# Performance work log

Hardware: AMD Instinct MI355X
Metric: run time of the kernel (lower is better)

The kernel has to match this reference:

```python
import jax, jax.numpy as jnp
import numpy as np

RADIUS = 5          # box-filter radius -> 11x11 kernel
TEMP = 0.5          # multinomial temperature
NSAMP = 5           # sampling_num
EPS = 1e-6
BN_EPS = 1e-5


def _conv(x, w, stride=1, padding=0, groups=1):
    return jax.lax.conv_general_dilated(
        x, w, window_strides=(stride, stride),
        padding=[(padding, padding), (padding, padding)],
        feature_group_count=groups,
        dimension_numbers=("NCHW", "OIHW", "NCHW"))


def custom_conv(x, w, key, stride=1, padding=0):
    """conv2d with cosine-activation regularization (bias=False path)."""
    B = x.shape[0]
    Cout = w.shape[0]
    # all-ones 'norm' conv on x*x
    x_norm = jnp.sqrt(_conv(x * x, jnp.ones_like(w), stride, padding))
    y = _conv(x, w, stride, padding)
    w_norm = jnp.sqrt(jnp.sum(w * w, axis=(1, 2, 3)))  # per-out-channel Frobenius norm
    cosine = y / (w_norm[None, :, None, None] + EPS) / (x_norm + EPS)
    # 11x11 depthwise box filter
    k = 2 * RADIUS + 1
    dw = jnp.ones((Cout, 1, k, k), x.dtype)
    cosine_mean = _conv(cosine, dw, 1, RADIUS, groups=Cout) / (k * k)
    H, W = cosine.shape[2], cosine.shape[3]
    # multinomial(NSAMP, exp(cosine/TEMP)) counts, no_grad in original
    logits = jax.lax.stop_gradient(cosine).reshape(B, Cout, H * W) / TEMP
    idx = jax.random.categorical(key, logits, axis=-1, shape=(NSAMP, B, Cout))
    bi = jnp.broadcast_to(jnp.arange(B)[None, :, None], (NSAMP, B, Cout))
    ci = jnp.broadcast_to(jnp.arange(Cout)[None, None, :], (NSAMP, B, Cout))
    mask = jnp.zeros((B, Cout, H * W), x.dtype).at[bi, ci, idx].add(1.0)
    cm = cosine_mean.reshape(B, Cout, H * W)
    act = ((mask * cm).sum(-1) / mask.sum(-1)).mean()
    return y, act


def batchnorm(x, g, b):
    # training-mode batch statistics (biased variance), like nn.BatchNorm2d
    m = x.mean(axis=(0, 2, 3), keepdims=True)
    v = x.var(axis=(0, 2, 3), keepdims=True)
    return (x - m) / jnp.sqrt(v + BN_EPS) * g[None, :, None, None] + b[None, :, None, None]


def setup_inputs() -> dict:
    key = jax.random.key(0)
    ks = jax.random.split(key, 10)
    x = jax.random.normal(ks[0], (16, 256, 56, 56), jnp.float32)
    w1 = jax.random.normal(ks[1], (64, 256, 1, 1), jnp.float32) * 0.05
    w2 = jax.random.normal(ks[2], (64, 64, 3, 3), jnp.float32) * 0.05
    w3 = jax.random.normal(ks[3], (256, 64, 1, 1), jnp.float32) * 0.05
    g1 = 1.0 + 0.05 * jax.random.normal(ks[4], (64,), jnp.float32)
    b1 = 0.05 * jax.random.normal(ks[5], (64,), jnp.float32)
    g2 = 1.0 + 0.05 * jax.random.normal(ks[6], (64,), jnp.float32)
    b2 = 0.05 * jax.random.normal(ks[7], (64,), jnp.float32)
    g3 = 1.0 + 0.05 * jax.random.normal(ks[8], (256,), jnp.float32)
    b3 = 0.05 * jax.random.normal(ks[9], (256,), jnp.float32)
    return {"x": x, "w1": w1, "w2": w2, "w3": w3,
            "g1": g1, "b1": b1, "g2": g2, "b2": b2, "g3": g3, "b3": b3}


def reference(x, w1, w2, w3, g1, b1, g2, b2, g3, b3):
    k0, k1, k2 = jax.random.split(jax.random.key(42), 3)
    acc = jnp.asarray(0.0, x.dtype)
    out, a = custom_conv(x, w1, k0)           # conv1x1
    acc = acc + a
    out = jax.nn.relu(batchnorm(out, g1, b1))
    out, a = custom_conv(out, w2, k1, padding=1)  # conv3x3, stride 1
    acc = acc + a
    out = jax.nn.relu(batchnorm(out, g2, b2))
    out, a = custom_conv(out, w3, k2)         # conv1x1 expand
    acc = acc + a
    out = batchnorm(out, g3, b3)
    out = jax.nn.relu(out + x)                # identity shortcut (downsample=None)
    return out, acc
```

## Files before the change

kernel.cpp:

```cpp
#include <hip/hip_runtime.h>
#include <stdint.h>
#include <math.h>

#define HW 3136
#define NPIX 50176

typedef __attribute__((ext_vector_type(8))) short bf16x8;
typedef __attribute__((ext_vector_type(4))) float f32x4;
#define MFMA16(a, b, c) __builtin_amdgcn_mfma_f32_16x16x32_bf16(a, b, c, 0, 0, 0)

__device__ __forceinline__ unsigned short f2bf(float f) {
  unsigned u = __float_as_uint(f);
  u = (u + 0x7fffu + ((u >> 16) & 1u)) >> 16;
  return (unsigned short)u;
}
__device__ __forceinline__ unsigned pk2(float a, float b) {
  return (unsigned)f2bf(a) | ((unsigned)f2bf(b) << 16);
}
__device__ __forceinline__ float bf2f(unsigned short h) {
  return __uint_as_float(((unsigned)h) << 16);
}

#define ROTL32(v, r) __builtin_rotateleft32((uint32_t)(v), (r))

__host__ __device__ inline void threefry2x32(uint32_t k0, uint32_t k1,
                                             uint32_t x0, uint32_t x1,
                                             uint32_t& o0, uint32_t& o1) {
  uint32_t k2 = k0 ^ k1 ^ 0x1BD11BDAu;
  x0 += k0; x1 += k1;
  x0 += x1; x1 = ROTL32(x1, 13); x1 ^= x0;
  x0 += x1; x1 = ROTL32(x1, 15); x1 ^= x0;
  x0 += x1; x1 = ROTL32(x1, 26); x1 ^= x0;
  x0 += x1; x1 = ROTL32(x1, 6);  x1 ^= x0;
  x0 += k1; x1 += k2 + 1u;
  x0 += x1; x1 = ROTL32(x1, 17); x1 ^= x0;
  x0 += x1; x1 = ROTL32(x1, 29); x1 ^= x0;
  x0 += x1; x1 = ROTL32(x1, 16); x1 ^= x0;
  x0 += x1; x1 = ROTL32(x1, 24); x1 ^= x0;
  x0 += k2; x1 += k0 + 2u;
  x0 += x1; x1 = ROTL32(x1, 13); x1 ^= x0;
  x0 += x1; x1 = ROTL32(x1, 15); x1 ^= x0;
  x0 += x1; x1 = ROTL32(x1, 26); x1 ^= x0;
  x0 += x1; x1 = ROTL32(x1, 6);  x1 ^= x0;
  x0 += k0; x1 += k1 + 3u;
  x0 += x1; x1 = ROTL32(x1, 17); x1 ^= x0;
  x0 += x1; x1 = ROTL32(x1, 29); x1 ^= x0;
  x0 += x1; x1 = ROTL32(x1, 16); x1 ^= x0;
  x0 += x1; x1 = ROTL32(x1, 24); x1 ^= x0;
  x0 += k1; x1 += k2 + 4u;
  x0 += x1; x1 = ROTL32(x1, 13); x1 ^= x0;
  x0 += x1; x1 = ROTL32(x1, 15); x1 ^= x0;
  x0 += x1; x1 = ROTL32(x1, 26); x1 ^= x0;
  x0 += x1; x1 = ROTL32(x1, 6);  x1 ^= x0;
  x0 += k2; x1 += k0 + 5u;
  o0 = x0; o1 = x1;
}

#define TF5_R(r)                                            \
  _Pragma("unroll") for (int i = 0; i < 5; ++i) {           \
    x0[i] += x1[i]; x1[i] = ROTL32(x1[i], r) ^ x0[i];       \
  }
#define TF5_INJ(a, b)                                       \
  _Pragma("unroll") for (int i = 0; i < 5; ++i) {           \
    x0[i] += (a); x1[i] += (b);                             \
  }
__device__ __forceinline__ void threefry5(uint32_t k0, uint32_t k1,
    const uint32_t xa[5], const uint32_t xb[5], uint32_t oa[5], uint32_t ob[5]) {
  uint32_t k2 = k0 ^ k1 ^ 0x1BD11BDAu;
  uint32_t x0[5], x1[5];
  #pragma unroll
  for (int i = 0; i < 5; ++i) { x0[i] = xa[i] + k0; x1[i] = xb[i] + k1; }
  TF5_R(13) TF5_R(15) TF5_R(26) TF5_R(6)  TF5_INJ(k1, k2 + 1u)
  TF5_R(17) TF5_R(29) TF5_R(16) TF5_R(24) TF5_INJ(k2, k0 + 2u)
  TF5_R(13) TF5_R(15) TF5_R(26) TF5_R(6)  TF5_INJ(k0, k1 + 3u)
  TF5_R(17) TF5_R(29) TF5_R(16) TF5_R(24) TF5_INJ(k1, k2 + 4u)
  TF5_R(13) TF5_R(15) TF5_R(26) TF5_R(6)  TF5_INJ(k2, k0 + 5u)
  #pragma unroll
  for (int i = 0; i < 5; ++i) { oa[i] = x0[i]; ob[i] = x1[i]; }
}

#define NLN2F -0.6931471805599453f
#define NEG2LOG2E -2.8853900817779268f
__device__ __forceinline__ float exp_draw(uint32_t bits) {
  float u = __uint_as_float((bits >> 9) | 0x3f800000u) - 1.0f;
  u = fmaxf(u, 1.17549435e-38f);
  return NLN2F * __log2f(u);
}

template <int NT>
__device__ void sample5_body(const unsigned short* __restrict__ CS,
    float* __restrict__ acc, uint32_t key0, uint32_t key1, int BC, float scale,
    int u, unsigned* kmin, float* wsum) {
  const int v = u + (BC >> 1);
  const uint32_t sC = (uint32_t)BC * (uint32_t)HW;
  const uint32_t halfn = sC * 2u + (sC >> 1);
  const unsigned short* rowU = CS + (size_t)u * HW;
  const unsigned short* rowV = CS + (size_t)v * HW;
  const int tid = threadIdx.x;
  const int lane = tid & 63;

  if (tid < 10) { kmin[tid] = 0xFFFFFFFFu; wsum[tid] = 0.f; }

  unsigned bk[10];
  #pragma unroll
  for (int k = 0; k < 10; ++k) bk[k] = 0xFFFFFFFFu;

  const uint32_t baseU0 = (uint32_t)u * (uint32_t)HW;
  const uint32_t baseV0 = (uint32_t)v * (uint32_t)HW;
  for (int p = tid; p < HW; p += NT) {
    float wu = __builtin_amdgcn_exp2f(bf2f(rowU[p]) * NEG2LOG2E);
    float wv = __builtin_amdgcn_exp2f(bf2f(rowV[p]) * NEG2LOG2E);
    uint32_t eU = baseU0 + (uint32_t)p;
    uint32_t eV = baseV0 + (uint32_t)p;
    uint32_t xa[5] = {eU, eU + sC, eU + 2 * sC, eV, eV + sC};
    uint32_t xb[5] = {eU + halfn, eU + sC + halfn, eU + 2 * sC + halfn,
                      eV + halfn, eV + sC + halfn};
    uint32_t oa[5], ob[5];
    threefry5(key0, key1, xa, xb, oa, ob);
    uint32_t wds[10] = {oa[0], oa[1], oa[2], ob[3], ob[4],
                        oa[3], oa[4], ob[0], ob[1], ob[2]};
    #pragma unroll
    for (int k = 0; k < 10; ++k) {
      float s = exp_draw(wds[k]) * (k < 5 ? wu : wv);
      unsigned key = (__float_as_uint(s) & 0xFFFFF000u) | (unsigned)p;
      bk[k] = bk[k] < key ? bk[k] : key;
    }
  }

  __syncthreads();
  #pragma unroll
  for (int k = 0; k < 10; ++k) {
    unsigned kv = bk[k];
    #pragma unroll
    for (int o = 32; o; o >>= 1) {
      unsigned ov = __shfl_xor(kv, o);
      kv = kv < ov ? kv : ov;
    }
    if (lane == 0) atomicMin(&kmin[k], kv);
  }
  __syncthreads();

  for (int idx = tid; idx < 1210; idx += NT) {
    int win = idx / 121, j = idx - win * 121;
    int bidx = (int)(kmin[win] & 0xFFFu);
    int py = bidx / 56, px = bidx % 56;
    int yy = py + j / 11 - 5, xx = px + j % 11 - 5;
    if (yy >= 0 && yy < 56 && xx >= 0 && xx < 56) {
      const unsigned short* row = (win < 5) ? rowU : rowV;
      atomicAdd(&wsum[win], bf2f(row[yy * 56 + xx]));
    }
  }
  __syncthreads();
  if (tid == 0) {
    float t = 0.f;
    #pragma unroll
    for (int k = 0; k < 10; ++k) t += wsum[k];
    atomicAdd(acc, t * scale);
  }
}

template <int NT>
__global__ __launch_bounds__(NT) void sample5_k(const unsigned short* __restrict__ CS,
    float* __restrict__ acc, uint32_t key0, uint32_t key1, int BC, float scale) {
  __shared__ unsigned kmin[10];
  __shared__ float wsum[10];
  sample5_body<NT>(CS, acc, key0, key1, BC, scale, blockIdx.x, kmin, wsum);
}

template <int NT>
__device__ void sample5_half_argmin(const unsigned short* __restrict__ CS,
    uint32_t key0, uint32_t key1, int BC, int u, int half,
    unsigned* __restrict__ outk, unsigned* kmin) {
  const int v = u + (BC >> 1);
  const uint32_t sC = (uint32_t)BC * (uint32_t)HW;
  const uint32_t halfn = sC * 2u + (sC >> 1);
  const unsigned short* rowU = CS + (size_t)u * HW;
  const unsigned short* rowV = CS + (size_t)v * HW;
  const int tid = threadIdx.x;
  const int lane = tid & 63;

  if (tid < 10) kmin[tid] = 0xFFFFFFFFu;

  unsigned bk[10];
  #pragma unroll
  for (int k = 0; k < 10; ++k) bk[k] = 0xFFFFFFFFu;

  const uint32_t baseU0 = (uint32_t)u * (uint32_t)HW;
  const uint32_t baseV0 = (uint32_t)v * (uint32_t)HW;
  const int pEnd = (half + 1) * (HW / 2);
  for (int p = half * (HW / 2) + tid; p < pEnd; p += NT) {
    float wu = __builtin_amdgcn_exp2f(bf2f(rowU[p]) * NEG2LOG2E);
    float wv = __builtin_amdgcn_exp2f(bf2f(rowV[p]) * NEG2LOG2E);
    uint32_t eU = baseU0 + (uint32_t)p;
    uint32_t eV = baseV0 + (uint32_t)p;
    uint32_t xa[5] = {eU, eU + sC, eU + 2 * sC, eV, eV + sC};
    uint32_t xb[5] = {eU + halfn, eU + sC + halfn, eU + 2 * sC + halfn,
                      eV + halfn, eV + sC + halfn};
    uint32_t oa[5], ob[5];
    threefry5(key0, key1, xa, xb, oa, ob);
    uint32_t wds[10] = {oa[0], oa[1], oa[2], ob[3], ob[4],
                        oa[3], oa[4], ob[0], ob[1], ob[2]};
    #pragma unroll
    for (int k = 0; k < 10; ++k) {
      float s = exp_draw(wds[k]) * (k < 5 ? wu : wv);
      unsigned key = (__float_as_uint(s) & 0xFFFFF000u) | (unsigned)p;
      bk[k] = bk[k] < key ? bk[k] : key;
    }
  }

  __syncthreads();
  #pragma unroll
  for (int k = 0; k < 10; ++k) {
    unsigned kv = bk[k];
    #pragma unroll
    for (int o = 32; o; o >>= 1) {
      unsigned ov = __shfl_xor(kv, o);
      kv = kv < ov ? kv : ov;
    }
    if (lane == 0) atomicMin(&kmin[k], kv);
  }
  __syncthreads();
  if (tid < 10) outk[tid] = kmin[tid];
}

__device__ __forceinline__ void final_chunk(int chunk,
    const unsigned short* __restrict__ Y3, const float* __restrict__ X,
    const float* __restrict__ sc, const float* __restrict__ sh,
    float* __restrict__ out) {
  size_t i = ((size_t)chunk * 256 + threadIdx.x) * 4;
  int c = (int)((i / HW) % 256);
  float a = sc[c], d = sh[c];
  uint2 yd = *(const uint2*)&Y3[i];
  float4 xv = *(const float4*)&X[i];
  float4 r;
  r.x = fmaxf(0.f, fmaf(bf2f((unsigned short)(yd.x & 0xffff)), a, d) + xv.x);
  r.y = fmaxf(0.f, fmaf(bf2f((unsigned short)(yd.x >> 16)),    a, d) + xv.y);
  r.z = fmaxf(0.f, fmaf(bf2f((unsigned short)(yd.y & 0xffff)), a, d) + xv.z);
  r.w = fmaxf(0.f, fmaf(bf2f((unsigned short)(yd.y >> 16)),    a, d) + xv.w);
  *(float4*)&out[i] = r;
}

__global__ __launch_bounds__(256, 8) void mega_argmin_k(
    const unsigned short* __restrict__ CS1, const unsigned short* __restrict__ CS2,
    const unsigned short* __restrict__ CS3,
    const unsigned short* __restrict__ Y3, const float* __restrict__ X,
    const float* __restrict__ sc, const float* __restrict__ sh,
    float* __restrict__ out, unsigned* __restrict__ bkmin,
    uint32_t A0, uint32_t A1, uint32_t A2, uint32_t B0, uint32_t B1, uint32_t B2,
    int pairStart, int finb) {
  __shared__ unsigned kmin[10];
  const int g = blockIdx.x;
  if (g < finb)
    for (int cc = g; cc < 12544; cc += finb)
      final_chunk(cc, Y3, X, sc, sh, out);
  const int lp = g >> 1, half = g & 1;
  const int pi = pairStart + lp;
  const unsigned short* CSp; int u; uint32_t k0, k1; int BC;
  if (pi < 512)       { CSp = CS1; u = pi;        k0 = A0; k1 = A1; BC = 1024; }
  else if (pi < 1024) { CSp = CS2; u = pi - 512;  k0 = A2; k1 = B0; BC = 1024; }
  else                { CSp = CS3; u = pi - 1024; k0 = B1; k1 = B2; BC = 4096; }
  sample5_half_argmin<256>(CSp, k0, k1, BC, u, half, bkmin + (size_t)g * 10, kmin);
}

__global__ __launch_bounds__(256) void combine_k(
    const unsigned short* __restrict__ CS1, const unsigned short* __restrict__ CS2,
    const unsigned short* __restrict__ CS3,
    const unsigned* __restrict__ bkmin, float* __restrict__ psum,
    float s64, float s256, int pairStart) {
  __shared__ unsigned kmin[10];
  __shared__ float wsum[10];
  const int tid = threadIdx.x, lane = tid & 63, wv = tid >> 6;
  const int rp = blockIdx.x;
  const int pi = pairStart + rp;
  const unsigned short* rowU; const unsigned short* rowV; float scale;
  if (pi < 512) {
    rowU = CS1 + (size_t)pi * HW; rowV = CS1 + (size_t)(pi + 512) * HW; scale = s64;
  } else if (pi < 1024) {
    int u = pi - 512;
    rowU = CS2 + (size_t)u * HW; rowV = CS2 + (size_t)(u + 512) * HW; scale = s64;
  } else {
    int u = pi - 1024;
    rowU = CS3 + (size_t)u * HW; rowV = CS3 + (size_t)(u + 2048) * HW; scale = s256;
  }
  if (tid < 10) {
    unsigned a = bkmin[(size_t)(2 * rp) * 10 + tid];
    unsigned b = bkmin[(size_t)(2 * rp + 1) * 10 + tid];
    kmin[tid] = a < b ? a : b;
  }
  __syncthreads();
  for (int win = wv; win < 10; win += 4) {
    int bidx = (int)(kmin[win] & 0xFFFu);
    int py = bidx / 56, px = bidx % 56;
    const unsigned short* row = (win < 5) ? rowU : rowV;
    float s = 0.f;
    for (int j = lane; j < 121; j += 64) {
      int yy = py + j / 11 - 5, xx = px + j % 11 - 5;
      if (yy >= 0 && yy < 56 && xx >= 0 && xx < 56)
        s += bf2f(row[yy * 56 + xx]);
    }
    #pragma unroll
    for (int o = 32; o; o >>= 1) s += __shfl_xor(s, o);
    if (lane == 0) wsum[win] = s;
  }
  __syncthreads();
  if (tid == 0) {
    float t = 0.f;
    #pragma unroll
    for (int k = 0; k < 10; ++k) t += wsum[k];
    psum[rp] = t * scale;
  }
}

__global__ __launch_bounds__(256) void acc_write_k(const float* __restrict__ psum,
    const float* __restrict__ acc, float* __restrict__ out, int n) {
  __shared__ float W[4];
  const int tid = threadIdx.x, lane = tid & 63, wv = tid >> 6;
  float s = 0.f;
  for (int i = tid; i < n; i += 256) s += psum[i];
  #pragma unroll
  for (int o = 32; o; o >>= 1) s += __shfl_xor(s, o);
  if (lane == 0) W[wv] = s;
  __syncthreads();
  if (tid == 0) out[12845056] = W[0] + W[1] + W[2] + W[3] + acc[0];
}

__global__ void wprep_k(const float* __restrict__ w1, const float* __restrict__ w2,
                        const float* __restrict__ w3, float* __restrict__ invwn,
                        unsigned short* __restrict__ W1b, unsigned short* __restrict__ W2tb,
                        unsigned short* __restrict__ W3b) {
  int i = blockIdx.x * 256 + threadIdx.x;
  if (i < 16384) {
    W1b[i] = f2bf(w1[i]);
  } else if (i < 53248) {
    int o = i - 16384;
    int co = o / 576, r = o % 576, tap = r >> 6, ci = r & 63;
    W2tb[o] = f2bf(w2[co * 576 + ci * 9 + tap]);
  } else if (i < 69632) {
    int o = i - 53248;
    W3b[o] = f2bf(w3[o]);
  } else {
    int t = i - 69632;
    if (t < 64) {
      float s = 0.f;
      for (int k = 0; k < 256; k++) { float v = w1[t * 256 + k]; s = fmaf(v, v, s); }
      invwn[t] = 1.0f / (sqrtf(s) + 1e-6f);
    } else if (t < 128) {
      int c = t - 64; float s = 0.f;
      for (int k = 0; k < 576; k++) { float v = w2[c * 576 + k]; s = fmaf(v, v, s); }
      invwn[t] = 1.0f / (sqrtf(s) + 1e-6f);
    } else if (t < 384) {
      int c = t - 128; float s = 0.f;
      for (int k = 0; k < 64; k++) { float v = w3[c * 64 + k]; s = fmaf(v, v, s); }
      invwn[t] = 1.0f / (sqrtf(s) + 1e-6f);
    }
  }
}

__global__ __launch_bounds__(256) void bn_fin(const float* __restrict__ Sp,
    const float* __restrict__ Qp, const float* __restrict__ g,
    const float* __restrict__ b, float* __restrict__ sc, float* __restrict__ sh,
    int nblk) {
  const int c = blockIdx.x, tid = threadIdx.x;
  const float* rs = Sp + (size_t)c * nblk;
  const float* rq = Qp + (size_t)c * nblk;
  float s = 0.f, q = 0.f;
  for (int i = tid; i < nblk; i += 256) { s += rs[i]; q += rq[i]; }
  #pragma unroll
  for (int o = 32; o; o >>= 1) { s += __shfl_xor(s, o); q += __shfl_xor(q, o); }
  __shared__ float S[4], Q[4];
  int lane = tid & 63, wave = tid >> 6;
  if (lane == 0) { S[wave] = s; Q[wave] = q; }
  __syncthreads();
  if (tid == 0) {
    float st = S[0] + S[1] + S[2] + S[3];
    float qt = Q[0] + Q[1] + Q[2] + Q[3];
    float mean = st * (1.0f / (float)NPIX);
    float var = qt * (1.0f / (float)NPIX) - mean * mean;
    float sv = g[c] / sqrtf(var + 1e-5f);
    sc[c] = sv; sh[c] = b[c] - mean * sv;
  }
}

__global__ __launch_bounds__(256) void conv1_mfma(
    const float* __restrict__ X, const unsigned short* __restrict__ Wb,
    const float* __restrict__ invwn, unsigned short* __restrict__ Y1,
    unsigned short* __restrict__ CS, float* __restrict__ Sp, float* __restrict__ Qp) {
#define ST1 264
#define NB1 784
  __shared__ __align__(16) unsigned short bq[64 * ST1];
  __shared__ float sqp[4][64];
  __shared__ float ixn[64];
  const int p0 = blockIdx.x * 64, b = blockIdx.y;
  const int bid = b * 49 + blockIdx.x;
  const int tid = threadIdx.x;
  const int lane = tid & 63, wave = tid >> 6;
  const int m = lane & 15, quad = lane >> 4;
  const int co0 = wave * 16;
  const float* Xb = X + (size_t)b * 256 * HW + p0;

  bf16x8 afr[8];
  const unsigned short* wrow = Wb + (co0 + m) * 256 + quad * 8;
  #pragma unroll
  for (int k = 0; k < 8; ++k) afr[k] = *(const bf16x8*)(wrow + k * 32);

  {
    const int px = tid & 63, rg = tid >> 6;
    float sq = 0.f;
    #pragma unroll
    for (int it = 0; it < 16; ++it) {
      int ci = rg * 64 + it * 4;
      float v0 = Xb[(size_t)(ci + 0) * HW + px];
      float v1 = Xb[(size_t)(ci + 1) * HW + px];
      float v2 = Xb[(size_t)(ci + 2) * HW + px];
      float v3 = Xb[(size_t)(ci + 3) * HW + px];
      sq += v0 * v0 + v1 * v1 + v2 * v2 + v3 * v3;
      *(uint2*)&bq[px * ST1 + ci] = make_uint2(pk2(v0, v1), pk2(v2, v3));
    }
    sqp[rg][px] = sq;
  }
  __syncthreads();
  if (tid < 64)
    ixn[tid] = 1.0f / (sqrtf(sqp[0][tid] + sqp[1][tid] + sqp[2][tid] + sqp[3][tid]) + 1e-6f);
  __syncthreads();

  f32x4 acc[4];
  #pragma unroll
  for (int nt = 0; nt < 4; ++nt) acc[nt] = (f32x4)0.f;
  #pragma unroll
  for (int nt = 0; nt < 4; ++nt) {
    const unsigned short* brow = &bq[(nt * 16 + m) * ST1 + quad * 8];
    #pragma unroll
    for (int k = 0; k < 8; ++k) {
      bf16x8 bfrag = *(const bf16x8*)(brow + k * 32);
      acc[nt] = MFMA16(afr[k], bfrag, acc[nt]);
    }
  }

  float s[4] = {0, 0, 0, 0}, q[4] = {0, 0, 0, 0};
  #pragma unroll
  for (int nt = 0; nt < 4; ++nt) {
    int px = nt * 16 + m;
    size_t bp = (size_t)b * HW + p0 + px;
    float ix = ixn[px];
    *(uint2*)&Y1[bp * 64 + co0 + quad * 4] =
        make_uint2(pk2(acc[nt][0], acc[nt][1]), pk2(acc[nt][2], acc[nt][3]));
    #pragma unroll
    for (int r = 0; r < 4; ++r) {
      int co = co0 + quad * 4 + r;
      float v = acc[nt][r];
      CS[((size_t)b * 64 + co) * HW + p0 + px] = f2bf(v * invwn[co] * ix);
      s[r] += v; q[r] = fmaf(v, v, q[r]);
    }
  }
  #pragma unroll
  for (int r = 0; r < 4; ++r) {
    float ss = s[r], qq = q[r];
    #pragma unroll
    for (int o = 8; o; o >>= 1) { ss += __shfl_xor(ss, o); qq += __shfl_xor(qq, o); }
    if (m == 0) {
      int co = co0 + quad * 4 + r;
      Sp[(size_t)co * NB1 + bid] = ss; Qp[(size_t)co * NB1 + bid] = qq;
    }
  }
#undef NB1
#undef ST1
}

__global__ __launch_bounds__(256) void conv2_mfma(
    const unsigned short* __restrict__ Y1, const unsigned short* __restrict__ W2tb,
    const float* __restrict__ invwn,
    const float* __restrict__ sc1, const float* __restrict__ sh1,
    unsigned short* __restrict__ Y2, unsigned short* __restrict__ CS,
    float* __restrict__ Sp, float* __restrict__ Qp) {
#define STW 72
#define NB2 896
  __shared__ __align__(16) unsigned short ts[3 * 66 * STW];
  __shared__ float scl[64], shl[64];
  __shared__ float spart[3 * 56];
  const int h = blockIdx.x, b = blockIdx.y;
  const int bid = b * 56 + h;
  const int tid = threadIdx.x;
  const int lane = tid & 63, wave = tid >> 6;
  const int m = lane & 15, quad = lane >> 4;
  const int co0 = wave * 16;
  if (tid < 64) { scl[tid] = sc1[tid]; shl[tid] = sh1[tid]; }

  bf16x8 afr[18];
  #pragma unroll
  for (int ks = 0; ks < 18; ++ks)
    afr[ks] = *(const bf16x8*)(W2tb + (co0 + m) * 576 + ks * 32 + quad * 8);
  __syncthreads();

  for (int l = tid; l < 6336; l += 256) {
    int cp = l & 31, cc = (l >> 5) % 66, dy = l / 2112;
    int yy = h - 1 + dy, xx = cc - 1;
    unsigned pkv = 0u;
    if (yy >= 0 && yy < 56 && xx >= 0 && xx < 56) {
      unsigned d = *(const unsigned*)&Y1[((size_t)b * HW + yy * 56 + xx) * 64 + cp * 2];
      float v0 = bf2f((unsigned short)(d & 0xffff));
      float v1 = bf2f((unsigned short)(d >> 16));
      v0 = fmaxf(0.f, fmaf(v0, scl[cp * 2], shl[cp * 2]));
      v1 = fmaxf(0.f, fmaf(v1, scl[cp * 2 + 1], shl[cp * 2 + 1]));
      pkv = pk2(v0, v1);
    }
    *(unsigned*)&ts[(dy * 66 + cc) * STW + cp * 2] = pkv;
  }
  __syncthreads();

  if (tid < 168) {
    int dy = tid / 56, x = tid - dy * 56;
    const unsigned* row = (const unsigned*)&ts[(dy * 66 + x + 1) * STW];
    float s = 0.f;
    #pragma unroll
    for (int j = 0; j < 32; ++j) {
      unsigned d = row[j];
      float v0 = bf2f((unsigned short)(d & 0xffff));
      float v1 = bf2f((unsigned short)(d >> 16));
      s = fmaf(v0, v0, s); s = fmaf(v1, v1, s);
    }
    spart[tid] = s;
  }
  __syncthreads();

  f32x4 acc[4];
  #pragma unroll
  for (int nt = 0; nt < 4; ++nt) acc[nt] = (f32x4)0.f;
  #pragma unroll
  for (int nt = 0; nt < 4; ++nt) {
    #pragma unroll
    for (int ks = 0; ks < 18; ++ks) {
      int tap = ks >> 1, half = ks & 1;
      int dy = tap / 3, dx = tap % 3;
      bf16x8 bfrag = *(const bf16x8*)&ts[(dy * 66 + nt * 16 + m + dx) * STW + half * 32 + quad * 8];
      acc[nt] = MFMA16(afr[ks], bfrag, acc[nt]);
    }
  }

  float s[4] = {0, 0, 0, 0}, q[4] = {0, 0, 0, 0};
  #pragma unroll
  for (int nt = 0; nt < 4; ++nt) {
    int px = nt * 16 + m;
    bool valid = px < 56;
    int pix = h * 56 + px;
    if (valid) {
      float tot = 0.f;
      #pragma unroll
      for (int dy = 0; dy < 3; ++dy) {
        #pragma unroll
        for (int dx = -1; dx <= 1; ++dx) {
          int xx = px + dx;
          if (xx >= 0 && xx < 56) tot += spart[dy * 56 + xx];
        }
      }
      float ix = 1.0f / (sqrtf(tot) + 1e-6f);
      size_t bp = (size_t)b * HW + pix;
      *(uint2*)&Y2[bp * 64 + co0 + quad * 4] =
          make_uint2(pk2(acc[nt][0], acc[nt][1]), pk2(acc[nt][2], acc[nt][3]));
      #pragma unroll
      for (int r = 0; r < 4; ++r) {
        int co = co0 + quad * 4 + r;
        CS[((size_t)b * 64 + co) * HW + pix] = f2bf(acc[nt][r] * invwn[co] * ix);
      }
    }
    #pragma unroll
    for (int r = 0; r < 4; ++r) {
      float v = valid ? acc[nt][r] : 0.f;
      s[r] += v; q[r] = fmaf(v, v, q[r]);
    }
  }
  #pragma unroll
  for (int r = 0; r < 4; ++r) {
    float ss = s[r], qq = q[r];
    #pragma unroll
    for (int o = 8; o; o >>= 1) { ss += __shfl_xor(ss, o); qq += __shfl_xor(qq, o); }
    if (m == 0) {
      int co = co0 + quad * 4 + r;
      Sp[(size_t)co * NB2 + bid] = ss; Qp[(size_t)co * NB2 + bid] = qq;
    }
  }
#undef NB2
#undef STW
}

__global__ __launch_bounds__(256) void conv3_mfma(
    const unsigned short* __restrict__ Y2, const unsigned short* __restrict__ W3b,
    const float* __restrict__ invwn,
    const float* __restrict__ sc2, const float* __restrict__ sh2,
    unsigned short* __restrict__ Y3, unsigned short* __restrict__ CS,
    float* __restrict__ Sp, float* __restrict__ Qp) {
#define ST3 72
#define NB3 784
  __shared__ __align__(16) unsigned short bq[64 * ST3];
  __shared__ float scl[64], shl[64], sqp[4][64], ixn[64];
  const int p0 = blockIdx.x * 64, b = blockIdx.y;
  const int bid = b * 49 + blockIdx.x;
  const int tid = threadIdx.x;
  const int lane = tid & 63, wave = tid >> 6;
  const int m = lane & 15, quad = lane >> 4;
  const int co0 = wave * 64;
  if (tid < 64) { scl[tid] = sc2[tid]; shl[tid] = sh2[tid]; }

  bf16x8 afr[4][2];
  #pragma unroll
  for (int mt = 0; mt < 4; ++mt)
    #pragma unroll
    for (int k = 0; k < 2; ++k)
      afr[mt][k] = *(const bf16x8*)(W3b + (co0 + mt * 16 + m) * 64 + k * 32 + quad * 8);
  __syncthreads();

  {
    const int cp = tid & 31, pxg = tid >> 5;
    #pragma unroll
    for (int it = 0; it < 8; ++it) {
      int px = pxg * 8 + it;
      unsigned d = *(const unsigned*)&Y2[((size_t)b * HW + p0 + px) * 64 + cp * 2];
      float v0 = bf2f((unsigned short)(d & 0xffff));
      float v1 = bf2f((unsigned short)(d >> 16));
      v0 = fmaxf(0.f, fmaf(v0, scl[cp * 2], shl[cp * 2]));
      v1 = fmaxf(0.f, fmaf(v1, scl[cp * 2 + 1], shl[cp * 2 + 1]));
      *(unsigned*)&bq[px * ST3 + cp * 2] = pk2(v0, v1);
    }
  }
  __syncthreads();
  {
    const int px = tid & 63, hh = tid >> 6;
    const unsigned short* row = &bq[px * ST3 + hh * 16];
    float sq = 0.f;
    #pragma unroll
    for (int e = 0; e < 16; ++e) { float v = bf2f(row[e]); sq = fmaf(v, v, sq); }
    sqp[hh][px] = sq;
  }
  __syncthreads();
  if (tid < 64)
    ixn[tid] = 1.0f / (sqrtf(sqp[0][tid] + sqp[1][tid] + sqp[2][tid] + sqp[3][tid]) + 1e-6f);
  __syncthreads();

  f32x4 acc[4][4];
  #pragma unroll
  for (int mt = 0; mt < 4; ++mt)
    #pragma unroll
    for (int nt = 0; nt < 4; ++nt) acc[mt][nt] = (f32x4)0.f;
  #pragma unroll
  for (int nt = 0; nt < 4; ++nt) {
    const unsigned short* brow = &bq[(nt * 16 + m) * ST3 + quad * 8];
    bf16x8 b0 = *(const bf16x8*)(brow);
    bf16x8 b1 = *(const bf16x8*)(brow + 32);
    #pragma unroll
    for (int mt = 0; mt < 4; ++mt) {
      acc[mt][nt] = MFMA16(afr[mt][0], b0, acc[mt][nt]);
      acc[mt][nt] = MFMA16(afr[mt][1], b1, acc[mt][nt]);
    }
  }

  #pragma unroll
  for (int mt = 0; mt < 4; ++mt) {
    float s[4] = {0, 0, 0, 0}, q[4] = {0, 0, 0, 0};
    #pragma unroll
    for (int nt = 0; nt < 4; ++nt) {
      int px = nt * 16 + m;
      float ix = ixn[px];
      #pragma unroll
      for (int r = 0; r < 4; ++r) {
        int co = co0 + mt * 16 + quad * 4 + r;
        float v = acc[mt][nt][r];
        size_t off = ((size_t)b * 256 + co) * HW + p0 + px;
        Y3[off] = f2bf(v);
        CS[off] = f2bf(v * invwn[co] * ix);
        s[r] += v; q[r] = fmaf(v, v, q[r]);
      }
    }
    #pragma unroll
    for (int r = 0; r < 4; ++r) {
      float ss = s[r], qq = q[r];
      #pragma unroll
      for (int o = 8; o; o >>= 1) { ss += __shfl_xor(ss, o); qq += __shfl_xor(qq, o); }
      if (m == 0) {
        int co = co0 + mt * 16 + quad * 4 + r;
        Sp[(size_t)co * NB3 + bid] = ss; Qp[(size_t)co * NB3 + bid] = qq;
      }
    }
  }
#undef NB3
#undef ST3
}

extern "C" void kernel_launch(void* const* d_in, const int* in_sizes, int n_in,
                              void* d_out, int out_size, void* d_ws, size_t ws_size,
                              hipStream_t stream) {
  (void)in_sizes; (void)n_in; (void)out_size;
  const float* x  = (const float*)d_in[0];
  const float* w1 = (const float*)d_in[1];
  const float* w2 = (const float*)d_in[2];
  const float* w3 = (const float*)d_in[3];
  const float* g1 = (const float*)d_in[4];
  const float* b1 = (const float*)d_in[5];
  const float* g2 = (const float*)d_in[6];
  const float* b2 = (const float*)d_in[7];
  const float* g3 = (const float*)d_in[8];
  const float* b3 = (const float*)d_in[9];
  float* out = (float*)d_out;
  float* ws = (float*)d_ws;

  size_t o = 0;
  unsigned short* y3b  = (unsigned short*)(ws + o); o += 6422528;
  unsigned short* cos3 = (unsigned short*)(ws + o); o += 6422528;
  unsigned short* CSb  = (unsigned short*)(ws + o); o += 1605632;
  unsigned short* y1b  = (unsigned short*)(ws + o); o += 1605632;
  unsigned short* y2b  = (unsigned short*)(ws + o); o += 1605632;
  unsigned short* W1b  = (unsigned short*)(ws + o); o += 8192;
  unsigned short* W2tb = (unsigned short*)(ws + o); o += 18432;
  unsigned short* W3b  = (unsigned short*)(ws + o); o += 8192;
  float* invwn = ws + o; o += 384;
  float* Sp1 = ws + o; o += 64 * 784;   float* Qp1 = ws + o; o += 64 * 784;
  float* Sp2 = ws + o; o += 64 * 896;   float* Qp2 = ws + o; o += 64 * 896;
  float* Sp3 = ws + o; o += 256 * 784;  float* Qp3 = ws + o; o += 256 * 784;
  float* acc = ws + o; o += 1;
  unsigned* bkmin = (unsigned*)(ws + o); o += 61440;
  float* psum = ws + o; o += 3072;
  float* sc1 = ws + o; o += 64;  float* sh1 = ws + o; o += 64;
  float* sc2 = ws + o; o += 64;  float* sh2 = ws + o; o += 64;
  float* sc3 = ws + o; o += 256; float* sh3 = ws + o; o += 256;

  const bool big = ws_size >= (o + 1605632) * sizeof(float);
  unsigned short* CS2b = big ? (unsigned short*)(ws + o) : CSb;

  hipMemsetAsync(acc, 0, sizeof(float), stream);

  uint32_t A0, B0, A1, B1, A2, B2;
  threefry2x32(0u, 42u, 0u, 3u, A0, B0);
  threefry2x32(0u, 42u, 1u, 4u, A1, B1);
  threefry2x32(0u, 42u, 2u, 5u, A2, B2);

  const float scale64  = 1.0f / (121.0f * 5.0f * 1024.0f);
  const float scale256 = 1.0f / (121.0f * 5.0f * 4096.0f);

  wprep_k<<<274, 256, 0, stream>>>(w1, w2, w3, invwn, W1b, W2tb, W3b);

  conv1_mfma<<<dim3(49, 16), 256, 0, stream>>>(x, W1b, invwn, y1b, CSb, Sp1, Qp1);
  bn_fin<<<64, 256, 0, stream>>>(Sp1, Qp1, g1, b1, sc1, sh1, 784);
  if (!big)
    sample5_k<512><<<512, 512, 0, stream>>>(CSb, acc, A0, A1, 1024, scale64);
  conv2_mfma<<<dim3(56, 16), 256, 0, stream>>>(
      y1b, W2tb, invwn + 64, sc1, sh1, y2b, CS2b, Sp2, Qp2);
  bn_fin<<<64, 256, 0, stream>>>(Sp2, Qp2, g2, b2, sc2, sh2, 896);
  if (!big)
    sample5_k<512><<<512, 512, 0, stream>>>(CS2b, acc, A2, B0, 1024, scale64);
  conv3_mfma<<<dim3(49, 16), 256, 0, stream>>>(
      y2b, W3b, invwn + 128, sc2, sh2, y3b, cos3, Sp3, Qp3);
  bn_fin<<<256, 256, 0, stream>>>(Sp3, Qp3, g3, b3, sc3, sh3, 784);

  if (big) {
    mega_argmin_k<<<6144, 256, 0, stream>>>(
        CSb, CS2b, cos3, y3b, x, sc3, sh3, out, bkmin,
        A0, A1, A2, B0, B1, B2, 0, 512);
    combine_k<<<3072, 256, 0, stream>>>(
        CSb, CS2b, cos3, bkmin, psum, scale64, scale256, 0);
    acc_write_k<<<1, 256, 0, stream>>>(psum, acc, out, 3072);
  } else {
    mega_argmin_k<<<4096, 256, 0, stream>>>(
        CSb, CS2b, cos3, y3b, x, sc3, sh3, out, bkmin,
        A0, A1, A2, B0, B1, B2, 1024, 512);
    combine_k<<<2048, 256, 0, stream>>>(
        CSb, CS2b, cos3, bkmin, psum, scale64, scale256, 1024);
    acc_write_k<<<1, 256, 0, stream>>>(psum, acc, out, 2048);
  }
}
```

Baseline: 365.2 us.

## Fuse box-filter window sums into argmin blocks and stage conv3 stores via LDS

Each half-argmin block now computes the 11x11 window sums for both of its local winners and writes the keys and sums to the workspace. The combine kernel becomes a tiny per-pair select-and-sum over those results instead of 3072 blocks that re-read the cosine rows. Separately, conv3's epilogue stages Y3 and the cosine output through shared memory so global writes are 16-byte vectorized rows instead of scattered 2-byte stores. The trade-off is twice the window-sum work (both halves compute it), a larger bkmin buffer, and extra LDS plus barriers in conv3.

```diff
diff --git a/kernel.cpp b/kernel.cpp
--- a/kernel.cpp
+++ b/kernel.cpp
@@ -170,14 +170,14 @@
 template <int NT>
 __device__ void sample5_half_argmin(const unsigned short* __restrict__ CS,
     uint32_t key0, uint32_t key1, int BC, int u, int half,
-    unsigned* __restrict__ outk, unsigned* kmin) {
+    unsigned* __restrict__ outk, unsigned* kmin, float* wsum) {
   const int v = u + (BC >> 1);
   const uint32_t sC = (uint32_t)BC * (uint32_t)HW;
   const uint32_t halfn = sC * 2u + (sC >> 1);
   const unsigned short* rowU = CS + (size_t)u * HW;
   const unsigned short* rowV = CS + (size_t)v * HW;
   const int tid = threadIdx.x;
-  const int lane = tid & 63;
+  const int lane = tid & 63, wv = tid >> 6;
 
   if (tid < 10) kmin[tid] = 0xFFFFFFFFu;
 
@@ -190,7 +190,7 @@
   const int pEnd = (half + 1) * (HW / 2);
   for (int p = half * (HW / 2) + tid; p < pEnd; p += NT) {
     float wu = __builtin_amdgcn_exp2f(bf2f(rowU[p]) * NEG2LOG2E);
-    float wv = __builtin_amdgcn_exp2f(bf2f(rowV[p]) * NEG2LOG2E);
+    float wv2 = __builtin_amdgcn_exp2f(bf2f(rowV[p]) * NEG2LOG2E);
     uint32_t eU = baseU0 + (uint32_t)p;
     uint32_t eV = baseV0 + (uint32_t)p;
     uint32_t xa[5] = {eU, eU + sC, eU + 2 * sC, eV, eV + sC};
@@ -202,7 +202,7 @@
                         oa[3], oa[4], ob[0], ob[1], ob[2]};
     #pragma unroll
     for (int k = 0; k < 10; ++k) {
-      float s = exp_draw(wds[k]) * (k < 5 ? wu : wv);
+      float s = exp_draw(wds[k]) * (k < 5 ? wu : wv2);
       unsigned key = (__float_as_uint(s) & 0xFFFFF000u) | (unsigned)p;
       bk[k] = bk[k] < key ? bk[k] : key;
     }
@@ -220,7 +220,26 @@
     if (lane == 0) atomicMin(&kmin[k], kv);
   }
   __syncthreads();
-  if (tid < 10) outk[tid] = kmin[tid];
+
+  for (int win = wv; win < 10; win += 4) {
+    int bidx = (int)(kmin[win] & 0xFFFu);
+    int py = bidx / 56, px = bidx % 56;
+    const unsigned short* row = (win < 5) ? rowU : rowV;
+    float s = 0.f;
+    for (int j = lane; j < 121; j += 64) {
+      int yy = py + j / 11 - 5, xx = px + j % 11 - 5;
+      if (yy >= 0 && yy < 56 && xx >= 0 && xx < 56)
+        s += bf2f(row[yy * 56 + xx]);
+    }
+    #pragma unroll
+    for (int o = 32; o; o >>= 1) s += __shfl_xor(s, o);
+    if (lane == 0) wsum[win] = s;
+  }
+  __syncthreads();
+  if (tid < 10) {
+    outk[tid] = kmin[tid];
+    outk[10 + tid] = __float_as_uint(wsum[tid]);
+  }
 }
 
 __device__ __forceinline__ void final_chunk(int chunk,
@@ -249,6 +268,7 @@
     uint32_t A0, uint32_t A1, uint32_t A2, uint32_t B0, uint32_t B1, uint32_t B2,
     int pairStart, int finb) {
   __shared__ unsigned kmin[10];
+  __shared__ float wsum[10];
   const int g = blockIdx.x;
   if (g < finb)
     for (int cc = g; cc < 12544; cc += finb)
@@ -259,56 +279,25 @@
   if (pi < 512)       { CSp = CS1; u = pi;        k0 = A0; k1 = A1; BC = 1024; }
   else if (pi < 1024) { CSp = CS2; u = pi - 512;  k0 = A2; k1 = B0; BC = 1024; }
   else                { CSp = CS3; u = pi - 1024; k0 = B1; k1 = B2; BC = 4096; }
-  sample5_half_argmin<256>(CSp, k0, k1, BC, u, half, bkmin + (size_t)g * 10, kmin);
+  sample5_half_argmin<256>(CSp, k0, k1, BC, u, half,
+                           bkmin + (size_t)g * 20, kmin, wsum);
 }
 
 __global__ __launch_bounds__(256) void combine_k(
-    const unsigned short* __restrict__ CS1, const unsigned short* __restrict__ CS2,
-    const unsigned short* __restrict__ CS3,
-    const unsigned* __restrict__ bkmin, float* __restrict__ psum,
-    float s64, float s256, int pairStart) {
-  __shared__ unsigned kmin[10];
-  __shared__ float wsum[10];
-  const int tid = threadIdx.x, lane = tid & 63, wv = tid >> 6;
-  const int rp = blockIdx.x;
-  const int pi = pairStart + rp;
-  const unsigned short* rowU; const unsigned short* rowV; float scale;
-  if (pi < 512) {
-    rowU = CS1 + (size_t)pi * HW; rowV = CS1 + (size_t)(pi + 512) * HW; scale = s64;
-  } else if (pi < 1024) {
-    int u = pi - 512;
-    rowU = CS2 + (size_t)u * HW; rowV = CS2 + (size_t)(u + 512) * HW; scale = s64;
-  } else {
-    int u = pi - 1024;
-    rowU = CS3 + (size_t)u * HW; rowV = CS3 + (size_t)(u + 2048) * HW; scale = s256;
-  }
-  if (tid < 10) {
-    unsigned a = bkmin[(size_t)(2 * rp) * 10 + tid];
-    unsigned b = bkmin[(size_t)(2 * rp + 1) * 10 + tid];
-    kmin[tid] = a < b ? a : b;
-  }
-  __syncthreads();
-  for (int win = wv; win < 10; win += 4) {
-    int bidx = (int)(kmin[win] & 0xFFFu);
-    int py = bidx / 56, px = bidx % 56;
-    const unsigned short* row = (win < 5) ? rowU : rowV;
-    float s = 0.f;
-    for (int j = lane; j < 121; j += 64) {
-      int yy = py + j / 11 - 5, xx = px + j % 11 - 5;
-      if (yy >= 0 && yy < 56 && xx >= 0 && xx < 56)
-        s += bf2f(row[yy * 56 + xx]);
-    }
-    #pragma unroll
-    for (int o = 32; o; o >>= 1) s += __shfl_xor(s, o);
-    if (lane == 0) wsum[win] = s;
-  }
-  __syncthreads();
-  if (tid == 0) {
-    float t = 0.f;
-    #pragma unroll
-    for (int k = 0; k < 10; ++k) t += wsum[k];
-    psum[rp] = t * scale;
-  }
+    const unsigned* __restrict__ bk, float* __restrict__ psum,
+    float s64, float s256, int pairStart, int nPairs) {
+  int rp = blockIdx.x * 256 + threadIdx.x;
+  if (rp >= nPairs) return;
+  const unsigned* h0 = bk + (size_t)(2 * rp) * 20;
+  const unsigned* h1 = bk + (size_t)(2 * rp + 1) * 20;
+  float t = 0.f;
+  #pragma unroll
+  for (int w = 0; w < 10; ++w) {
+    unsigned k0 = h0[w], k1 = h1[w];
+    t += __uint_as_float(k0 < k1 ? h0[10 + w] : h1[10 + w]);
+  }
+  int pi = pairStart + rp;
+  psum[rp] = t * (pi < 1024 ? s64 : s256);
 }
 
 __global__ __launch_bounds__(256) void acc_write_k(const float* __restrict__ psum,
@@ -591,6 +580,7 @@
 #define ST3 72
 #define NB3 784
   __shared__ __align__(16) unsigned short bq[64 * ST3];
+  __shared__ __align__(16) unsigned short stC[64 * ST3];
   __shared__ float scl[64], shl[64], sqp[4][64], ixn[64];
   const int p0 = blockIdx.x * 64, b = blockIdx.y;
   const int bid = b * 49 + blockIdx.x;
@@ -657,15 +647,9 @@
     float s[4] = {0, 0, 0, 0}, q[4] = {0, 0, 0, 0};
     #pragma unroll
     for (int nt = 0; nt < 4; ++nt) {
-      int px = nt * 16 + m;
-      float ix = ixn[px];
       #pragma unroll
       for (int r = 0; r < 4; ++r) {
-        int co = co0 + mt * 16 + quad * 4 + r;
         float v = acc[mt][nt][r];
-        size_t off = ((size_t)b * 256 + co) * HW + p0 + px;
-        Y3[off] = f2bf(v);
-        CS[off] = f2bf(v * invwn[co] * ix);
         s[r] += v; q[r] = fmaf(v, v, q[r]);
       }
     }
@@ -678,6 +662,38 @@
         int co = co0 + mt * 16 + quad * 4 + r;
         Sp[(size_t)co * NB3 + bid] = ss; Qp[(size_t)co * NB3 + bid] = qq;
       }
+    }
+  }
+
+  #pragma unroll
+  for (int mt = 0; mt < 4; ++mt) {
+    __syncthreads();
+    #pragma unroll
+    for (int nt = 0; nt < 4; ++nt) {
+      int px = nt * 16 + m;
+      float ix = ixn[px];
+      #pragma unroll
+      for (int r = 0; r < 4; ++r) {
+        int cl = wave * 16 + quad * 4 + r;
+        int co = co0 + mt * 16 + quad * 4 + r;
+        float v = acc[mt][nt][r];
+        bq[cl * ST3 + px] = f2bf(v);
+        stC[cl * ST3 + px] = f2bf(v * invwn[co] * ix);
+      }
+    }
+    __syncthreads();
+    {
+      int cl = tid >> 2, pq = tid & 3;
+      int co = (cl >> 4) * 64 + mt * 16 + (cl & 15);
+      size_t off = ((size_t)b * 256 + co) * HW + p0 + pq * 16;
+      uint4 y0 = *(uint4*)&bq[cl * ST3 + pq * 16];
+      uint4 y1 = *(uint4*)&bq[cl * ST3 + pq * 16 + 8];
+      *(uint4*)&Y3[off] = y0;
+      *(uint4*)&Y3[off + 8] = y1;
+      uint4 c0 = *(uint4*)&stC[cl * ST3 + pq * 16];
+      uint4 c1 = *(uint4*)&stC[cl * ST3 + pq * 16 + 8];
+      *(uint4*)&CS[off] = c0;
+      *(uint4*)&CS[off + 8] = c1;
     }
   }
 #undef NB3
@@ -715,7 +731,7 @@
   float* Sp2 = ws + o; o += 64 * 896;   float* Qp2 = ws + o; o += 64 * 896;
   float* Sp3 = ws + o; o += 256 * 784;  float* Qp3 = ws + o; o += 256 * 784;
   float* acc = ws + o; o += 1;
-  unsigned* bkmin = (unsigned*)(ws + o); o += 61440;
+  unsigned* bkmin = (unsigned*)(ws + o); o += 122880;
   float* psum = ws + o; o += 3072;
   float* sc1 = ws + o; o += 64;  float* sh1 = ws + o; o += 64;
   float* sc2 = ws + o; o += 64;  float* sh2 = ws + o; o += 64;
@@ -753,15 +769,15 @@
     mega_argmin_k<<<6144, 256, 0, stream>>>(
         CSb, CS2b, cos3, y3b, x, sc3, sh3, out, bkmin,
         A0, A1, A2, B0, B1, B2, 0, 512);
-    combine_k<<<3072, 256, 0, stream>>>(
-        CSb, CS2b, cos3, bkmin, psum, scale64, scale256, 0);
+    combine_k<<<12, 256, 0, stream>>>(
+        bkmin, psum, scale64, scale256, 0, 3072);
     acc_write_k<<<1, 256, 0, stream>>>(psum, acc, out, 3072);
   } else {
     mega_argmin_k<<<4096, 256, 0, stream>>>(
         CSb, CS2b, cos3, y3b, x, sc3, sh3, out, bkmin,
         A0, A1, A2, B0, B1, B2, 1024, 512);
-    combine_k<<<2048, 256, 0, stream>>>(
-        CSb, CS2b, cos3, bkmin, psum, scale64, scale256, 1024);
+    combine_k<<<8, 256, 0, stream>>>(
+        bkmin, psum, scale64, scale256, 1024, 2048);
     acc_write_k<<<1, 256, 0, stream>>>(psum, acc, out, 2048);
   }
 }
```

Measured after the change: 374.2 us. +2.5%, slower.
